# Performance work log

Hardware: AMD Instinct MI355X
Metric: run time of the kernel (lower is better)

The kernel has to match this reference:

```python
import jax, jax.numpy as jnp
import numpy as np

B, N, C_IN, C_OUT, K = 4, 4096, 128, 128, 3
EPS = 1e-06
LAMBDA_MAX = 2.0  # compute_lambda_max=False and lambda_max=None -> 2.0


def setup_inputs() -> dict:
    key = jax.random.key(0)
    k1, k2, k3 = jax.random.split(key, 3)
    x = jax.random.normal(k1, (B, N, C_IN), dtype=jnp.float32)
    adj = jax.random.uniform(k2, (B, N, N), dtype=jnp.float32)
    W = jax.random.normal(k3, (C_OUT, K * C_IN), dtype=jnp.float32) * 0.05
    return {"x": x, "adj": adj, "W": W}


def reference(x, adj, W):
    # degree: sum over dim=1 of adj (matches torch adj.sum(dim=1).unsqueeze(-1))
    degree = jnp.sum(adj, axis=1)[:, :, None]          # [B, N, 1]
    lambda_ratio = 2.0 / (LAMBDA_MAX + EPS)

    def cheb_step(z):
        # lr * D * z - lr * A @ z - z, fused elementwise around one bmm
        return lambda_ratio * (degree * z - jnp.einsum('bnm,bmc->bnc', adj, z)) - z

    Z_list = [x, cheb_step(x)]
    for k in range(2, K):
        Z_list.append(2.0 * cheb_step(Z_list[k - 1]) - Z_list[k - 2])

    Z = jnp.stack(Z_list, axis=1)                      # [B, K, N, C]
    # replicate torch .view(B, N, -1) on contiguous [B, K, N, C]
    Z = Z.reshape(Z.shape[0], Z.shape[2], -1)          # [B, N, K*C]
    out = jnp.einsum('bnf,of->bno', Z, W)              # Linear, no bias
    return out
```

## Files before the change

kernel.cpp:

```cpp
#include <hip/hip_runtime.h>


#define NN 4096
#define CF 128
#define NC (NN * CF)
#define LRC 0.9999995f

typedef __attribute__((ext_vector_type(8))) short bf16x8;
typedef __attribute__((ext_vector_type(4))) float f32x4;

__device__ __forceinline__ unsigned short f2b(float f) {
    unsigned u = __float_as_uint(f);
    return (unsigned short)((u + 0x7FFFu + ((u >> 16) & 1u)) >> 16);
}

__global__ __launch_bounds__(256) void prep_cast(const float* __restrict__ adj,
                                                 unsigned short* __restrict__ adjB,
                                                 float* __restrict__ deg) {
    const int b = blockIdx.z;
    const size_t base = (size_t)b * NN * NN;
    const int n0 = blockIdx.x * 1024;
    const int m0 = blockIdx.y * 64;
    const int t = threadIdx.x;
    float4 s = make_float4(0.f, 0.f, 0.f, 0.f);
    const size_t col = (size_t)(n0 + t * 4);
    for (int m = 0; m < 64; ++m) {
        const size_t idx = base + (size_t)(m0 + m) * NN + col;
        const float4 v = *(const float4*)&adj[idx];
        s.x += v.x; s.y += v.y; s.z += v.z; s.w += v.w;
        ushort4 o;
        o.x = f2b(v.x); o.y = f2b(v.y); o.z = f2b(v.z); o.w = f2b(v.w);
        *(ushort4*)&adjB[idx] = o;
    }
    float* dp = deg + b * NN + n0 + t * 4;
    atomicAdd(dp + 0, s.x);
    atomicAdd(dp + 1, s.y);
    atomicAdd(dp + 2, s.z);
    atomicAdd(dp + 3, s.w);
}

__global__ __launch_bounds__(256) void transpose_x(const float* __restrict__ x,
                                                   unsigned short* __restrict__ xTb) {
    __shared__ float tile[64][65];
    const int b = blockIdx.z, m0 = blockIdx.x * 64, n0 = blockIdx.y * 64;
    const int t = threadIdx.x;
    const int c = t & 63, r4 = t >> 6;
    const float* xb = x + (size_t)b * NC;
#pragma unroll
    for (int i = 0; i < 16; ++i) {
        int r = i * 4 + r4;
        tile[r][c] = xb[(size_t)(m0 + r) * CF + n0 + c];
    }
    __syncthreads();
    unsigned short* xo = xTb + (size_t)b * NC + (size_t)n0 * NN + m0;
#pragma unroll
    for (int i = 0; i < 16; ++i) {
        int r = i * 4 + r4;
        xo[(size_t)r * NN + c] = f2b(tile[c][r]);
    }
}

__global__ __launch_bounds__(256) void wt_kernel(const float* __restrict__ W,
                                                 float* __restrict__ Wt) {
    const int idx = blockIdx.x * 256 + threadIdx.x;
    const int o = idx / 384;
    const int f = idx % 384;
    Wt[f * 128 + o] = W[idx];
}

template <int PHASE>
__global__ __launch_bounds__(256) void gemm_cheb(
    const unsigned short* __restrict__ adjB,
    const unsigned short* __restrict__ Bt,
    const float* __restrict__ x,
    const float* __restrict__ deg,
    float* __restrict__ Zf,
    unsigned short* __restrict__ z1Tb)
{
    const int t = threadIdx.x;
    const int w = t >> 6, lane = t & 63, q = lane >> 4, l16 = lane & 15;
    const int m0 = blockIdx.x * 64;
    const int b  = blockIdx.y;

    __shared__ __align__(16) short As[2][4096];
    __shared__ __align__(16) short Bs[2][8192];

    const int g  = t & 7;
    const int r0 = t >> 3;

    const unsigned short* ap = adjB + (size_t)b * NN * NN + (size_t)m0 * NN + g * 8;
    const unsigned short* bp = Bt   + (size_t)b * NC + g * 8;

    f32x4 acc[4][2];
#pragma unroll
    for (int i = 0; i < 4; ++i)
#pragma unroll
        for (int j = 0; j < 2; ++j) acc[i][j] = (f32x4)0.f;

    bf16x8 ar[2], br[4];
    ar[0] = *(const bf16x8*)(ap + (size_t)r0 * NN);
    ar[1] = *(const bf16x8*)(ap + (size_t)(r0 + 32) * NN);
#pragma unroll
    for (int i = 0; i < 4; ++i)
        br[i] = *(const bf16x8*)(bp + (size_t)(r0 + 32 * i) * NN);

    {
        const int ra = r0, rb = r0 + 32;
        *(bf16x8*)&As[0][ra * 64 + ((g ^ (ra & 7)) << 3)] = ar[0];
        *(bf16x8*)&As[0][rb * 64 + ((g ^ (rb & 7)) << 3)] = ar[1];
#pragma unroll
        for (int i = 0; i < 4; ++i) {
            const int r = r0 + 32 * i;
            *(bf16x8*)&Bs[0][r * 64 + ((g ^ (r & 7)) << 3)] = br[i];
        }
    }

    int cur = 0;
    for (int it = 0; it < 64; ++it) {
        __syncthreads();
        if (it < 63) {
            const size_t kof = (size_t)(it + 1) * 64;
            ar[0] = *(const bf16x8*)(ap + (size_t)r0 * NN + kof);
            ar[1] = *(const bf16x8*)(ap + (size_t)(r0 + 32) * NN + kof);
#pragma unroll
            for (int i = 0; i < 4; ++i)
                br[i] = *(const bf16x8*)(bp + (size_t)(r0 + 32 * i) * NN + kof);
        }
#pragma unroll
        for (int kh = 0; kh < 2; ++kh) {
            bf16x8 af[4], bfr[2];
#pragma unroll
            for (int i = 0; i < 4; ++i) {
                const int ml = i * 16 + l16;
                af[i] = *(const bf16x8*)&As[cur][ml * 64 + ((((kh << 2) + q) ^ (ml & 7)) << 3)];
            }
#pragma unroll
            for (int j = 0; j < 2; ++j) {
                const int nl = w * 32 + j * 16 + l16;
                bfr[j] = *(const bf16x8*)&Bs[cur][nl * 64 + ((((kh << 2) + q) ^ (nl & 7)) << 3)];
            }
#pragma unroll
            for (int i = 0; i < 4; ++i)
#pragma unroll
                for (int j = 0; j < 2; ++j)
                    acc[i][j] = __builtin_amdgcn_mfma_f32_16x16x32_bf16(
                        af[i], bfr[j], acc[i][j], 0, 0, 0);
        }
        if (it < 63) {
            const int nxt = cur ^ 1;
            const int ra = r0, rb = r0 + 32;
            *(bf16x8*)&As[nxt][ra * 64 + ((g ^ (ra & 7)) << 3)] = ar[0];
            *(bf16x8*)&As[nxt][rb * 64 + ((g ^ (rb & 7)) << 3)] = ar[1];
#pragma unroll
            for (int i = 0; i < 4; ++i) {
                const int r = r0 + 32 * i;
                *(bf16x8*)&Bs[nxt][r * 64 + ((g ^ (r & 7)) << 3)] = br[i];
            }
            cur = nxt;
        }
    }

    const float* xb   = x + (size_t)b * NC;
    const float* degb = deg + b * NN;
    float* Z1 = Zf + (size_t)b * 2 * NC;

    if (PHASE == 0) {
        __syncthreads();
        short (*sh)[68] = (short(*)[68])(&Bs[0][0]);
#pragma unroll
        for (int i = 0; i < 4; ++i) {
#pragma unroll
            for (int r = 0; r < 4; ++r) {
                const int ml = i * 16 + q * 4 + r;
                const int m  = m0 + ml;
                const float d = degb[m];
#pragma unroll
                for (int j = 0; j < 2; ++j) {
                    const int n = w * 32 + j * 16 + l16;
                    const float xv = xb[(size_t)m * CF + n];
                    const float zz = LRC * (d * xv - acc[i][j][r]) - xv;
                    Z1[(size_t)m * CF + n] = zz;
                    sh[n][ml] = (short)f2b(zz);
                }
            }
        }
        __syncthreads();
        const int f  = t >> 1;
        const int h0 = (t & 1) * 32;
        unsigned short* zo = z1Tb + (size_t)b * NC + (size_t)f * NN + m0 + h0;
        const short* srow = &sh[f][h0];
#pragma unroll
        for (int v = 0; v < 8; ++v)
            ((ushort4*)zo)[v] = ((const ushort4*)srow)[v];
    } else {
        const float* Z1c = Z1;
        float* Z2 = Z1 + NC;
#pragma unroll
        for (int i = 0; i < 4; ++i) {
#pragma unroll
            for (int r = 0; r < 4; ++r) {
                const int m = m0 + i * 16 + q * 4 + r;
                const float d = degb[m];
#pragma unroll
                for (int j = 0; j < 2; ++j) {
                    const int n = w * 32 + j * 16 + l16;
                    const float xv  = xb[(size_t)m * CF + n];
                    const float z1v = Z1c[(size_t)m * CF + n];
                    Z2[(size_t)m * CF + n] =
                        2.f * (LRC * (d * z1v - acc[i][j][r]) - z1v) - xv;
                }
            }
        }
    }
}

__global__ __launch_bounds__(256) void gemm_final(const float* __restrict__ x,
                                                  const float* __restrict__ Zf,
                                                  const float* __restrict__ Wt,
                                                  float* __restrict__ out) {
    const int b = blockIdx.z;
    float* Cb = out + (size_t)b * NC;

    const int t = threadIdx.x;
    const int tx = t & 15, ty = t >> 4;
    const int m0 = blockIdx.y * 64, n0 = blockIdx.x * 64;

    __shared__ float Asm[16][68];
    __shared__ float Bsm[16][64];

    const int arow = t >> 2;
    const int ak4 = (t & 3) << 2;
    const int bk = t >> 4;
    const int bn4 = (t & 15) << 2;

    const float* xb = x + (size_t)b * NC;

    float4 acc[4];
    acc[0] = acc[1] = acc[2] = acc[3] = make_float4(0.f, 0.f, 0.f, 0.f);

    const float* bptr = Wt + (size_t)bk * 128 + n0 + bn4;

    auto aload = [&](int k) -> float4 {
        const unsigned G = (unsigned)(m0 + arow) * 384u + (unsigned)k;
        const int chunk = (int)(G >> 19);
        const unsigned rem = G & 524287u;
        const float* src = (chunk == 0) ? xb : (Zf + (size_t)(b * 2 + (chunk - 1)) * NC);
        return *(const float4*)&src[rem];
    };

    float4 av = aload(ak4);
    float4 bv = *(const float4*)bptr;

    for (int k0 = 0; k0 < 384; k0 += 16) {
        __syncthreads();
        Asm[ak4 + 0][arow] = av.x;
        Asm[ak4 + 1][arow] = av.y;
        Asm[ak4 + 2][arow] = av.z;
        Asm[ak4 + 3][arow] = av.w;
        *(float4*)&Bsm[bk][bn4] = bv;
        __syncthreads();
        if (k0 + 16 < 384) {
            av = aload(k0 + 16 + ak4);
            bv = *(const float4*)(bptr + (size_t)(k0 + 16) * 128);
        }
#pragma unroll
        for (int kk = 0; kk < 16; ++kk) {
            const float4 a = *(const float4*)&Asm[kk][ty << 2];
            const float4 bb = *(const float4*)&Bsm[kk][tx << 2];
            acc[0].x += a.x * bb.x; acc[0].y += a.x * bb.y; acc[0].z += a.x * bb.z; acc[0].w += a.x * bb.w;
            acc[1].x += a.y * bb.x; acc[1].y += a.y * bb.y; acc[1].z += a.y * bb.z; acc[1].w += a.y * bb.w;
            acc[2].x += a.z * bb.x; acc[2].y += a.z * bb.y; acc[2].z += a.z * bb.z; acc[2].w += a.z * bb.w;
            acc[3].x += a.w * bb.x; acc[3].y += a.w * bb.y; acc[3].z += a.w * bb.z; acc[3].w += a.w * bb.w;
        }
    }

    const int ncol = n0 + (tx << 2);
#pragma unroll
    for (int i = 0; i < 4; ++i) {
        const int m = m0 + (ty << 2) + i;
        *(float4*)&Cb[(size_t)m * 128 + ncol] = acc[i];
    }
}

extern "C" void kernel_launch(void* const* d_in, const int* in_sizes, int n_in,
                              void* d_out, int out_size, void* d_ws, size_t ws_size,
                              hipStream_t stream) {
    const float* x   = (const float*)d_in[0];
    const float* adj = (const float*)d_in[1];
    const float* W   = (const float*)d_in[2];
    float* out = (float*)d_out;

    char* ws = (char*)d_ws;
    unsigned short* adjB = (unsigned short*)ws;
    float* Zf            = (float*)(ws + 134217728u);
    unsigned short* xTb  = (unsigned short*)(ws + 150994944u);
    unsigned short* z1Tb = (unsigned short*)(ws + 155189248u);
    float* deg           = (float*)(ws + 159383552u);
    float* Wt            = (float*)(ws + 159449088u);

    hipMemsetAsync(deg, 0, 4 * NN * sizeof(float), stream);
    prep_cast<<<dim3(4, 64, 4), 256, 0, stream>>>(adj, adjB, deg);
    transpose_x<<<dim3(64, 2, 4), 256, 0, stream>>>(x, xTb);
    wt_kernel<<<192, 256, 0, stream>>>(W, Wt);

    gemm_cheb<0><<<dim3(64, 4), 256, 0, stream>>>(adjB, xTb, x, deg, Zf, z1Tb);
    gemm_cheb<1><<<dim3(64, 4), 256, 0, stream>>>(adjB, z1Tb, x, deg, Zf, z1Tb);

    gemm_final<<<dim3(2, 64, 4), 256, 0, stream>>>(x, Zf, Wt, out);
}
```

Baseline: 544.0 us.

## Halve gemm_cheb row tile, load B fragments directly to registers, swizzle blocks

```diff
diff --git a/kernel.cpp b/kernel.cpp
--- a/kernel.cpp
+++ b/kernel.cpp
@@ -24,13 +24,18 @@
     const int t = threadIdx.x;
     float4 s = make_float4(0.f, 0.f, 0.f, 0.f);
     const size_t col = (size_t)(n0 + t * 4);
-    for (int m = 0; m < 64; ++m) {
-        const size_t idx = base + (size_t)(m0 + m) * NN + col;
-        const float4 v = *(const float4*)&adj[idx];
-        s.x += v.x; s.y += v.y; s.z += v.z; s.w += v.w;
-        ushort4 o;
-        o.x = f2b(v.x); o.y = f2b(v.y); o.z = f2b(v.z); o.w = f2b(v.w);
-        *(ushort4*)&adjB[idx] = o;
+    for (int m = 0; m < 64; m += 4) {
+        float4 v[4];
+#pragma unroll
+        for (int u = 0; u < 4; ++u)
+            v[u] = *(const float4*)&adj[base + (size_t)(m0 + m + u) * NN + col];
+#pragma unroll
+        for (int u = 0; u < 4; ++u) {
+            s.x += v[u].x; s.y += v[u].y; s.z += v[u].z; s.w += v[u].w;
+            ushort4 o;
+            o.x = f2b(v[u].x); o.y = f2b(v[u].y); o.z = f2b(v[u].z); o.w = f2b(v[u].w);
+            *(ushort4*)&adjB[base + (size_t)(m0 + m + u) * NN + col] = o;
+        }
     }
     float* dp = deg + b * NN + n0 + t * 4;
     atomicAdd(dp + 0, s.x);
@@ -69,7 +74,7 @@
 }
 
 template <int PHASE>
-__global__ __launch_bounds__(256) void gemm_cheb(
+__global__ __launch_bounds__(256, 2) void gemm_cheb(
     const unsigned short* __restrict__ adjB,
     const unsigned short* __restrict__ Bt,
     const float* __restrict__ x,
@@ -79,96 +84,86 @@
 {
     const int t = threadIdx.x;
     const int w = t >> 6, lane = t & 63, q = lane >> 4, l16 = lane & 15;
-    const int m0 = blockIdx.x * 64;
-    const int b  = blockIdx.y;
-
-    __shared__ __align__(16) short As[2][4096];
-    __shared__ __align__(16) short Bs[2][8192];
-
-    const int g  = t & 7;
-    const int r0 = t >> 3;
-
-    const unsigned short* ap = adjB + (size_t)b * NN * NN + (size_t)m0 * NN + g * 8;
-    const unsigned short* bp = Bt   + (size_t)b * NC + g * 8;
-
-    f32x4 acc[4][2];
-#pragma unroll
-    for (int i = 0; i < 4; ++i)
+
+    const int bid = blockIdx.x;
+    const int swz = (bid & 7) * 64 + (bid >> 3);
+    const int b   = swz >> 7;
+    const int m0  = (swz & 127) * 32;
+
+    __shared__ __align__(16) short As[2][32 * 64];
+
+    const int rA = t >> 3, gA = t & 7;
+    const int awslot = rA * 64 + ((gA ^ (rA & 7)) << 3);
+    const unsigned short* ap = adjB + (size_t)b * NN * NN + (size_t)(m0 + rA) * NN + gA * 8;
+
+    const unsigned short* bp = Bt + (size_t)b * NC + (size_t)(w * 32 + l16) * NN + q * 8;
+
+    f32x4 acc[2][2];
+#pragma unroll
+    for (int i = 0; i < 2; ++i)
 #pragma unroll
         for (int j = 0; j < 2; ++j) acc[i][j] = (f32x4)0.f;
 
-    bf16x8 ar[2], br[4];
-    ar[0] = *(const bf16x8*)(ap + (size_t)r0 * NN);
-    ar[1] = *(const bf16x8*)(ap + (size_t)(r0 + 32) * NN);
-#pragma unroll
-    for (int i = 0; i < 4; ++i)
-        br[i] = *(const bf16x8*)(bp + (size_t)(r0 + 32 * i) * NN);
+    bf16x8 aw, afp;
+    bf16x8 bc0[2][2], bc1[2][2];
 
     {
-        const int ra = r0, rb = r0 + 32;
-        *(bf16x8*)&As[0][ra * 64 + ((g ^ (ra & 7)) << 3)] = ar[0];
-        *(bf16x8*)&As[0][rb * 64 + ((g ^ (rb & 7)) << 3)] = ar[1];
-#pragma unroll
-        for (int i = 0; i < 4; ++i) {
-            const int r = r0 + 32 * i;
-            *(bf16x8*)&Bs[0][r * 64 + ((g ^ (r & 7)) << 3)] = br[i];
-        }
-    }
-
-    int cur = 0;
-    for (int it = 0; it < 64; ++it) {
-        __syncthreads();
-        if (it < 63) {
-            const size_t kof = (size_t)(it + 1) * 64;
-            ar[0] = *(const bf16x8*)(ap + (size_t)r0 * NN + kof);
-            ar[1] = *(const bf16x8*)(ap + (size_t)(r0 + 32) * NN + kof);
-#pragma unroll
-            for (int i = 0; i < 4; ++i)
-                br[i] = *(const bf16x8*)(bp + (size_t)(r0 + 32 * i) * NN + kof);
-        }
-#pragma unroll
-        for (int kh = 0; kh < 2; ++kh) {
-            bf16x8 af[4], bfr[2];
-#pragma unroll
-            for (int i = 0; i < 4; ++i) {
-                const int ml = i * 16 + l16;
-                af[i] = *(const bf16x8*)&As[cur][ml * 64 + ((((kh << 2) + q) ^ (ml & 7)) << 3)];
-            }
-#pragma unroll
-            for (int j = 0; j < 2; ++j) {
-                const int nl = w * 32 + j * 16 + l16;
-                bfr[j] = *(const bf16x8*)&Bs[cur][nl * 64 + ((((kh << 2) + q) ^ (nl & 7)) << 3)];
-            }
-#pragma unroll
-            for (int i = 0; i < 4; ++i)
-#pragma unroll
-                for (int j = 0; j < 2; ++j)
-                    acc[i][j] = __builtin_amdgcn_mfma_f32_16x16x32_bf16(
-                        af[i], bfr[j], acc[i][j], 0, 0, 0);
-        }
-        if (it < 63) {
-            const int nxt = cur ^ 1;
-            const int ra = r0, rb = r0 + 32;
-            *(bf16x8*)&As[nxt][ra * 64 + ((g ^ (ra & 7)) << 3)] = ar[0];
-            *(bf16x8*)&As[nxt][rb * 64 + ((g ^ (rb & 7)) << 3)] = ar[1];
-#pragma unroll
-            for (int i = 0; i < 4; ++i) {
-                const int r = r0 + 32 * i;
-                *(bf16x8*)&Bs[nxt][r * 64 + ((g ^ (r & 7)) << 3)] = br[i];
-            }
-            cur = nxt;
-        }
-    }
+        const bf16x8 a0 = *(const bf16x8*)(ap);
+        aw = *(const bf16x8*)(ap + 64);
+#pragma unroll
+        for (int j = 0; j < 2; ++j)
+#pragma unroll
+            for (int kh = 0; kh < 2; ++kh)
+                bc0[j][kh] = *(const bf16x8*)(bp + (size_t)(j * 16) * NN + kh * 32);
+        *(bf16x8*)&As[0][awslot] = a0;
+    }
+
+#define CHEB_BODY(CUR, BCUR, BNXT)                                              \
+    {                                                                           \
+        __syncthreads();                                                        \
+        if (it + 2 < 64) afp = *(const bf16x8*)(ap + (size_t)(it + 2) * 64);    \
+        if (it + 1 < 64) {                                                      \
+            _Pragma("unroll") for (int j = 0; j < 2; ++j)                       \
+            _Pragma("unroll") for (int kh = 0; kh < 2; ++kh)                    \
+                BNXT[j][kh] = *(const bf16x8*)(bp + (size_t)(j * 16) * NN       \
+                                               + (size_t)(it + 1) * 64 + kh * 32); \
+        }                                                                       \
+        bf16x8 af[2][2];                                                        \
+        _Pragma("unroll") for (int i = 0; i < 2; ++i)                           \
+        _Pragma("unroll") for (int kh = 0; kh < 2; ++kh) {                      \
+            const int ml = i * 16 + l16;                                        \
+            const int ss = kh * 4 + q;                                          \
+            af[i][kh] = *(const bf16x8*)&As[CUR][ml * 64 + ((ss ^ (ml & 7)) << 3)]; \
+        }                                                                       \
+        _Pragma("unroll") for (int i = 0; i < 2; ++i)                           \
+        _Pragma("unroll") for (int j = 0; j < 2; ++j) {                         \
+            acc[i][j] = __builtin_amdgcn_mfma_f32_16x16x32_bf16(                \
+                af[i][0], BCUR[j][0], acc[i][j], 0, 0, 0);                      \
+            acc[i][j] = __builtin_amdgcn_mfma_f32_16x16x32_bf16(                \
+                af[i][1], BCUR[j][1], acc[i][j], 0, 0, 0);                      \
+        }                                                                       \
+        if (it + 1 < 64) {                                                      \
+            *(bf16x8*)&As[CUR ^ 1][awslot] = aw;                                \
+            aw = afp;                                                           \
+        }                                                                       \
+        ++it;                                                                   \
+    }
+
+    int it = 0;
+    while (it < 64) {
+        CHEB_BODY(0, bc0, bc1)
+        CHEB_BODY(1, bc1, bc0)
+    }
+#undef CHEB_BODY
 
     const float* xb   = x + (size_t)b * NC;
     const float* degb = deg + b * NN;
     float* Z1 = Zf + (size_t)b * 2 * NC;
 
-    if (PHASE == 0) {
-        __syncthreads();
-        short (*sh)[68] = (short(*)[68])(&Bs[0][0]);
-#pragma unroll
-        for (int i = 0; i < 4; ++i) {
+    if constexpr (PHASE == 0) {
+        __shared__ __align__(16) short sh[128][36];
+#pragma unroll
+        for (int i = 0; i < 2; ++i) {
 #pragma unroll
             for (int r = 0; r < 4; ++r) {
                 const int ml = i * 16 + q * 4 + r;
@@ -186,17 +181,17 @@
         }
         __syncthreads();
         const int f  = t >> 1;
-        const int h0 = (t & 1) * 32;
+        const int h0 = (t & 1) * 16;
         unsigned short* zo = z1Tb + (size_t)b * NC + (size_t)f * NN + m0 + h0;
         const short* srow = &sh[f][h0];
 #pragma unroll
-        for (int v = 0; v < 8; ++v)
+        for (int v = 0; v < 4; ++v)
             ((ushort4*)zo)[v] = ((const ushort4*)srow)[v];
     } else {
         const float* Z1c = Z1;
         float* Z2 = Z1 + NC;
 #pragma unroll
-        for (int i = 0; i < 4; ++i) {
+        for (int i = 0; i < 2; ++i) {
 #pragma unroll
             for (int r = 0; r < 4; ++r) {
                 const int m = m0 + i * 16 + q * 4 + r;
@@ -303,8 +298,8 @@
     transpose_x<<<dim3(64, 2, 4), 256, 0, stream>>>(x, xTb);
     wt_kernel<<<192, 256, 0, stream>>>(W, Wt);
 
-    gemm_cheb<0><<<dim3(64, 4), 256, 0, stream>>>(adjB, xTb, x, deg, Zf, z1Tb);
-    gemm_cheb<1><<<dim3(64, 4), 256, 0, stream>>>(adjB, z1Tb, x, deg, Zf, z1Tb);
+    gemm_cheb<0><<<512, 256, 0, stream>>>(adjB, xTb, x, deg, Zf, z1Tb);
+    gemm_cheb<1><<<512, 256, 0, stream>>>(adjB, z1Tb, x, deg, Zf, z1Tb);
 
     gemm_final<<<dim3(2, 64, 4), 256, 0, stream>>>(x, Zf, Wt, out);
 }
```

Result: slower. 567.7 us (+4.4%).
